# Optimization experiments

Measured on AMD Instinct MI355X. Metric: run time of the kernel, lower is better.

The kernel has to match this reference:

```python
import jax, jax.numpy as jnp
import numpy as np

B, TP, TH = 128, 128, 64
V, E, H, O = 50000, 300, 512, 3


def _lstm(x, lens, Wih, Whh, bih, bhh):
    # PyTorch LSTM, batch_first, gate order i,f,g,o; masked like pack_padded_sequence
    Bn, T, _ = x.shape
    Hn = Whh.shape[1]
    mask = jnp.arange(T)[None, :] < lens[:, None]  # [B,T]
    def step(carry, xt_mt):
        h, c = carry
        xt, mt = xt_mt  # [B,E], [B,1]
        g = xt @ Wih.T + h @ Whh.T + bih + bhh
        i, f, gg, o = jnp.split(g, 4, axis=-1)
        c_new = jax.nn.sigmoid(f) * c + jax.nn.sigmoid(i) * jnp.tanh(gg)
        h_new = jax.nn.sigmoid(o) * jnp.tanh(c_new)
        return (jnp.where(mt, h_new, h), jnp.where(mt, c_new, c)), jnp.where(mt, h_new, 0.0)
    z = jnp.zeros((Bn, Hn), x.dtype)
    _, hs = jax.lax.scan(step, (z, z), (jnp.swapaxes(x, 0, 1), jnp.swapaxes(mask, 0, 1)[..., None]))
    return jnp.swapaxes(hs, 0, 1)  # [B,T,H]


def _cell(x, h, c, Wih, Whh, bih, bhh):
    g = x @ Wih.T + h @ Whh.T + bih + bhh
    i, f, gg, o = jnp.split(g, 4, axis=-1)
    c_new = jax.nn.sigmoid(f) * c + jax.nn.sigmoid(i) * jnp.tanh(gg)
    h_new = jax.nn.sigmoid(o) * jnp.tanh(c_new)
    return h_new, c_new


def setup_inputs() -> dict:
    key = jax.random.key(0)
    ks = jax.random.split(key, 24)
    def unif(k, shape, fan):
        s = 1.0 / np.sqrt(fan)
        return jax.random.uniform(k, shape, jnp.float32, -s, s)
    inp = {}
    inp["premise"] = jax.random.randint(ks[0], (B, TP), 0, V, jnp.int32)
    inp["premise_len"] = jnp.full((B,), TP, jnp.int32)
    inp["hypothesis"] = jax.random.randint(ks[1], (B, TH), 0, V, jnp.int32)
    inp["hypothesis_len"] = jnp.full((B,), TH, jnp.int32)
    inp["embed_table"] = jax.random.normal(ks[2], (V, E), jnp.float32) * 0.1
    inp["embed_table"] = inp["embed_table"].at[0].set(0.0)  # padding_idx=0
    # premise LSTM
    inp["Wih_p"] = unif(ks[3], (4 * H, E), H); inp["Whh_p"] = unif(ks[4], (4 * H, H), H)
    inp["bih_p"] = unif(ks[5], (4 * H,), H); inp["bhh_p"] = unif(ks[6], (4 * H,), H)
    # hypothesis LSTM
    inp["Wih_h"] = unif(ks[7], (4 * H, E), H); inp["Whh_h"] = unif(ks[8], (4 * H, H), H)
    inp["bih_h"] = unif(ks[9], (4 * H,), H); inp["bhh_h"] = unif(ks[10], (4 * H,), H)
    # match LSTMCell (input 2H)
    inp["Wih_m"] = unif(ks[11], (4 * H, 2 * H), H); inp["Whh_m"] = unif(ks[12], (4 * H, H), H)
    inp["bih_m"] = unif(ks[13], (4 * H,), H); inp["bhh_m"] = unif(ks[14], (4 * H,), H)
    # attention
    inp["w_e"] = jax.random.uniform(ks[15], (H,), jnp.float32, 0.0, 1.0)
    inp["W_s"] = unif(ks[16], (H, H), H)
    inp["W_t"] = unif(ks[17], (H, H), H)
    inp["W_m"] = unif(ks[18], (H, H), H)
    inp["W_fc"] = unif(ks[19], (O, H), H)
    inp["b_fc"] = unif(ks[20], (O,), H)
    return inp


def reference(premise, premise_len, hypothesis, hypothesis_len, embed_table,
              Wih_p, Whh_p, bih_p, bhh_p, Wih_h, Whh_h, bih_h, bhh_h,
              Wih_m, Whh_m, bih_m, bhh_m, w_e, W_s, W_t, W_m, W_fc, b_fc):
    Bn = premise.shape[0]
    Hn = Whh_m.shape[1]
    p_emb = embed_table[premise]      # [B,Tp,E]
    h_emb = embed_table[hypothesis]   # [B,Th,E]
    h_s = _lstm(p_emb, premise_len, Wih_p, Whh_p, bih_p, bhh_p)      # [B,Tp,H]
    h_t = _lstm(h_emb, hypothesis_len, Wih_h, Whh_h, bih_h, bhh_h)   # [B,Th,H]
    Ws = jnp.einsum('bth,gh->btg', h_s, W_s)  # precompute w_s(h_s) once

    def step(carry, htk):
        h_m, c_m = carry
        q = htk @ W_t.T + h_m @ W_m.T                    # [B,H]
        s = jnp.tanh(Ws + q[:, None, :])                 # [B,Tp,H]
        e = s @ w_e                                      # [B,Tp]
        alpha = jax.nn.softmax(e, axis=1)                # softmax over premise positions
        a = jnp.einsum('bt,bth->bh', alpha, h_s)
        m_k = jnp.concatenate([a, htk], axis=1)          # [B,2H]
        h_m2, c_m2 = _cell(m_k, h_m, c_m, Wih_m, Whh_m, bih_m, bhh_m)
        return (h_m2, c_m2), h_m2

    z = jnp.zeros((Bn, Hn), h_s.dtype)
    _, hm_all = jax.lax.scan(step, (z, z), jnp.swapaxes(h_t, 0, 1))  # [Th,B,H]
    hm_all = jnp.swapaxes(hm_all, 0, 1)                              # [B,Th,H]
    idx = (hypothesis_len - 1).astype(jnp.int32)[:, None, None]
    last = jnp.take_along_axis(hm_all, idx, axis=1)[:, 0, :]         # last hidden per example
    return last @ W_fc.T + b_fc
```

## Files before the change

kernel.cpp:

```cpp
#include <hip/hip_runtime.h>
#include <hip/hip_bf16.h>

constexpr int BB = 128;
constexpr int TPp = 128;
constexpr int THh = 64;
constexpr int HH = 512;

constexpr size_t OFF_HS     = 0;
constexpr size_t SZ_HS      = (size_t)16384 * 512;
constexpr size_t OFF_HT     = OFF_HS + SZ_HS;
constexpr size_t SZ_HT      = (size_t)8192 * 512;
constexpr size_t OFF_WSM    = OFF_HT + SZ_HT;
constexpr size_t SZ_WSM     = (size_t)16384 * 512;
constexpr size_t OFF_XG_P   = OFF_WSM;
constexpr size_t OFF_XG_H   = OFF_WSM + (size_t)16 * 128 * 128 * 16;
constexpr size_t OFF_WIHT_P = OFF_WSM + SZ_WSM;
constexpr size_t SZ_WIHT    = (size_t)304 * 2048;
constexpr size_t OFF_WIHT_H = OFF_WIHT_P + SZ_WIHT;
constexpr size_t OFF_WHHT_P = OFF_WIHT_H + SZ_WIHT;
constexpr size_t OFF_WHHT_H = OFF_WHHT_P + (size_t)512 * 2048;
constexpr size_t OFF_WB1T   = OFF_WHHT_H + (size_t)512 * 2048;
constexpr size_t OFF_WIA    = OFF_WB1T + (size_t)2560 * 1024;
constexpr size_t OFF_WEF    = OFF_WIA + (size_t)2048 * 512;
constexpr size_t OFF_BM     = OFF_WEF + 512;
constexpr size_t OFF_HC_P   = OFF_BM + 2048;
constexpr size_t OFF_HC_H   = OFF_HC_P + 2 * (size_t)BB * HH;
constexpr size_t OFF_C_P    = OFF_HC_H + 2 * (size_t)BB * HH;
constexpr size_t OFF_C_H    = OFF_C_P + (size_t)BB * HH;
constexpr size_t OFF_Q      = OFF_C_H + (size_t)BB * HH;
constexpr size_t OFF_GH     = OFF_Q + (size_t)BB * HH;
constexpr size_t OFF_A      = OFF_GH + (size_t)BB * 2048;
constexpr size_t OFF_HM     = OFF_A + (size_t)BB * HH;
constexpr size_t OFF_CM     = OFF_HM + (size_t)BB * HH;
constexpr size_t OFF_LAST   = OFF_CM + (size_t)BB * HH;
constexpr size_t OFF_BARP   = OFF_LAST + (size_t)BB * HH;
constexpr size_t OFF_BARH   = OFF_BARP + 2560;
constexpr size_t OFF_BARF   = OFF_BARH + 2560;
constexpr size_t OFF_BARM   = OFF_BARF + 4352;
constexpr size_t WS_FLOATS  = OFF_BARM + 4352;

__device__ __forceinline__ float sigmf(float x) { return 1.0f / (1.0f + __expf(-x)); }
__device__ __forceinline__ float tanh_f(float x) {
  float e = __expf(-2.0f * fabsf(x));
  float r = (1.0f - e) / (1.0f + e);
  return copysignf(r, x);
}

__device__ __forceinline__ void gbarN(unsigned* bar, int ep, int base, int n) {
  __syncthreads();
  const int tid = threadIdx.x;
  const int rel = (int)blockIdx.x - base;
  if (tid == 0) {
    __threadfence();
    __hip_atomic_store(bar + (size_t)rel * 16, (unsigned)ep,
                       __ATOMIC_RELAXED, __HIP_MEMORY_SCOPE_AGENT);
  }
  if (rel == 0) {
    for (int s = tid; s < n; s += (int)blockDim.x) {
      while (__hip_atomic_load(bar + (size_t)s * 16,
                               __ATOMIC_RELAXED, __HIP_MEMORY_SCOPE_AGENT) < (unsigned)ep)
        __builtin_amdgcn_s_sleep(1);
    }
    __syncthreads();
    if (tid == 0)
      __hip_atomic_store(bar + (size_t)n * 16, (unsigned)ep,
                         __ATOMIC_RELAXED, __HIP_MEMORY_SCOPE_AGENT);
  } else if (tid == 0) {
    while (__hip_atomic_load(bar + (size_t)n * 16,
                             __ATOMIC_RELAXED, __HIP_MEMORY_SCOPE_AGENT) < (unsigned)ep)
      __builtin_amdgcn_s_sleep(1);
  }
  if (tid == 0) __threadfence();
  __syncthreads();
}

__global__ void k_diag(float* out, float v) {
  int i = blockIdx.x * 64 + threadIdx.x;
  if (i < BB * 3) out[i] = v;
}

__global__ __launch_bounds__(256) void k_prep(float* ws,
    const float* Wih_p, const float* bih_p, const float* bhh_p,
    const float* Wih_h, const float* bih_h, const float* bhh_h,
    const float* Whh_p, const float* Whh_h,
    const float* Whh_m, const float* Wih_m, const float* bih_m, const float* bhh_m,
    const float* W_m, const float* W_t, const float* w_e) {
  size_t gid = (size_t)blockIdx.x * 256 + threadIdx.x;
  if (gid < SZ_WIHT) {
    int k = (int)(gid >> 11), r = (int)(gid & 2047);
    float v = (k < 300) ? Wih_p[(size_t)r * 300 + k]
            : (k == 303) ? (bih_p[r] + bhh_p[r]) : 0.f;
    ws[OFF_WIHT_P + gid] = v;
    return;
  }
  gid -= SZ_WIHT;
  if (gid < SZ_WIHT) {
    int k = (int)(gid >> 11), r = (int)(gid & 2047);
    float v = (k < 300) ? Wih_h[(size_t)r * 300 + k]
            : (k == 303) ? (bih_h[r] + bhh_h[r]) : 0.f;
    ws[OFF_WIHT_H + gid] = v;
    return;
  }
  gid -= SZ_WIHT;
  const size_t NT = (size_t)512 * 2048;
  if (gid < NT) {
    int li = (int)(gid >> 13);
    int rem = (int)(gid & 8191);
    int k = rem >> 4, c = rem & 15;
    int jj = c >> 2, g = c & 3;
    ws[OFF_WHHT_P + gid] = Whh_p[(size_t)(g * 512 + li * 4 + jj) * 512 + k];
    return;
  }
  gid -= NT;
  if (gid < NT) {
    int li = (int)(gid >> 13);
    int rem = (int)(gid & 8191);
    int k = rem >> 4, c = rem & 15;
    int jj = c >> 2, g = c & 3;
    ws[OFF_WHHT_H + gid] = Whh_h[(size_t)(g * 512 + li * 4 + jj) * 512 + k];
    return;
  }
  gid -= NT;
  if (gid < (size_t)2560 * 1024) {
    int c = (int)(gid >> 10), k = (int)(gid & 1023);
    float v;
    if (c < 512) {
      v = (k < 512) ? W_m[(size_t)c * 512 + k] : W_t[(size_t)c * 512 + (k - 512)];
    } else {
      int p = c - 512;
      int j = p >> 2, g = p & 3;
      int r = g * 512 + j;
      v = (k < 512) ? Whh_m[(size_t)r * 512 + k] : Wih_m[(size_t)r * 1024 + k];
    }
    ws[OFF_WB1T + gid] = v;
    return;
  }
  gid -= (size_t)2560 * 1024;
  if (gid < (size_t)2048 * 512) {
    int c = (int)(gid >> 9), k = (int)(gid & 511);
    int j = c >> 2, g = c & 3;
    ws[OFF_WIA + gid] = Wih_m[((size_t)g * 512 + j) * 1024 + k];
    return;
  }
  gid -= (size_t)2048 * 512;
  if (gid < 512) { ws[OFF_WEF + gid] = w_e[gid]; return; }
  gid -= 512;
  if (gid < 2048) { ws[OFF_BM + gid] = bih_m[gid] + bhh_m[gid]; return; }
  gid -= 2048;
  if (gid < (size_t)393216) { ws[OFF_HC_P + gid] = 0.f; return; }
  gid -= 393216;
  if (gid < (size_t)131072) { ws[OFF_HM + gid] = 0.f; return; }
  gid -= 131072;
  if (gid < 11824) { ws[OFF_BARP + gid] = 0.f; return; }
}

__global__ __launch_bounds__(256) void k_gemm(const float* __restrict__ A,
                                              const float* __restrict__ Bw, int ldb, int Kdim,
                                              int N, float* __restrict__ C, int ntilesN) {
  __shared__ float As[16][68];
  __shared__ float Bs[16][68];
  const int tid = threadIdx.x;
  const int bid = blockIdx.x;
  const int tm = bid / ntilesN, tn = bid % ntilesN;
  const int m0 = tm * 64, n0 = tn * 64;
  const int tx = tid & 15, ty = tid >> 4;
  const int srow = tid >> 2, skc = (tid & 3) * 4;
  float acc[4][4] = {};
  const float* arowf = A + (size_t)(m0 + srow) * Kdim;
  const float* brow = Bw + (size_t)(n0 + srow) * ldb;
  for (int k0 = 0; k0 < Kdim; k0 += 16) {
    float4 v = *(const float4*)(arowf + k0 + skc);
    As[skc + 0][srow] = v.x; As[skc + 1][srow] = v.y;
    As[skc + 2][srow] = v.z; As[skc + 3][srow] = v.w;
#pragma unroll
    for (int i = 0; i < 4; i++) Bs[skc + i][srow] = brow[k0 + skc + i];
    __syncthreads();
#pragma unroll
    for (int kk = 0; kk < 16; kk++) {
      float4 a4 = *(float4*)&As[kk][ty * 4];
      float4 b4 = *(float4*)&Bs[kk][tx * 4];
      acc[0][0] += a4.x * b4.x; acc[0][1] += a4.x * b4.y; acc[0][2] += a4.x * b4.z; acc[0][3] += a4.x * b4.w;
      acc[1][0] += a4.y * b4.x; acc[1][1] += a4.y * b4.y; acc[1][2] += a4.y * b4.z; acc[1][3] += a4.y * b4.w;
      acc[2][0] += a4.z * b4.x; acc[2][1] += a4.z * b4.y; acc[2][2] += a4.z * b4.z; acc[2][3] += a4.z * b4.w;
      acc[3][0] += a4.w * b4.x; acc[3][1] += a4.w * b4.y; acc[3][2] += a4.w * b4.z; acc[3][3] += a4.w * b4.w;
    }
    __syncthreads();
  }
  const int m = m0 + ty * 4, n = n0 + tx * 4;
#pragma unroll
  for (int i = 0; i < 4; i++) {
    float4 o = {acc[i][0], acc[i][1], acc[i][2], acc[i][3]};
    *(float4*)&C[(size_t)(m + i) * N + n] = o;
  }
}

__global__ __launch_bounds__(512, 2) void k_lstm_mega(float* __restrict__ ws,
    const int* __restrict__ premise, const int* __restrict__ hyp,
    const int* __restrict__ plen, const int* __restrict__ hlen,
    const float* __restrict__ emb) {
  __shared__ float4 smem4[4096];
  float4* wlds4 = smem4;
  float4* hbuf4 = smem4 + 2048;
  float* xAs = (float*)(smem4 + 2048);
  float* xBs = xAs + 16 * 68;
  int* xTok = (int*)(xBs + 16 * 68);

  const int tid = threadIdx.x;
  const int bid = blockIdx.x;
  const int seq = bid >> 7;
  const int li = bid & 127;
  const int T = seq ? THh : TPp;
  const int* lens = seq ? hlen : plen;
  const float* wstk = ws + (seq ? OFF_WHHT_H : OFF_WHHT_P) + (size_t)li * 8192;
  float* hsout = ws + (seq ? OFF_HT : OFF_HS);
  float* hc = ws + (seq ? OFF_HC_H : OFF_HC_P);
  unsigned* barS = (unsigned*)(ws + (seq ? OFF_BARH : OFF_BARP));
  unsigned* barF = (unsigned*)(ws + OFF_BARF);
  const int sbase = seq ? 128 : 0;

  {
    const float4* src = (const float4*)wstk;
#pragma unroll
    for (int j2 = 0; j2 < 4; j2++) wlds4[tid + j2 * 512] = src[tid + j2 * 512];
  }
  const int w = tid >> 6, lane = tid & 63;
  const int cg = w & 3, bh = w >> 2;
  const int b = bh * 64 + lane;
  const int sw = b & 7;
  const int jcol = li * 4 + cg;
  const int len = lens[b];
  float c_r = 0.f, h_r = 0.f;
  int epS = 1, epF = 1;

  int sb[4], sk[4];
#pragma unroll
  for (int j2 = 0; j2 < 4; j2++) { int fi = tid + j2 * 512; sb[j2] = fi >> 4; sk[j2] = fi & 15; }

  for (int t = 0; t < TPp; t++) {
    if ((t & 15) == 0) {
      if (t > 0) { gbarN(barF, epF, 0, 256); epF++; }
      int ntl = (t < THh) ? 2048 : 1024;
      __syncthreads();
      for (int tile = bid; tile < ntl; tile += 256) {
        const int seqx = tile >> 10;
        const int u = tile & 1023;
        const int tm = u >> 5, tn = u & 31;
        const int m0 = tm * 64, n0 = tn * 64;
        const int Tx = seqx ? THh : TPp;
        const int* toks = seqx ? hyp : premise;
        const float* WX = ws + (seqx ? OFF_WIHT_H : OFF_WIHT_P);
        float* xg = ws + (seqx ? OFF_XG_H : OFF_XG_P);
        if (tid < 64) {
          int rr = m0 + tid;
          int tl = rr >> 7, bb = rr & 127;
          xTok[tid] = toks[(size_t)bb * Tx + t + tl];
        }
        __syncthreads();
        const int sr = tid & 63;
        const int sk2 = (tid >> 6) * 2;
        const int tx = tid & 15, ty = tid >> 4;
        float acc2[2][4] = {};
        for (int k0 = 0; k0 < 304; k0 += 16) {
          int tok = xTok[sr];
#pragma unroll
          for (int i = 0; i < 2; i++) {
            int kx = k0 + sk2 + i;
            float v = 0.f;
            if (kx < 300) v = emb[(size_t)tok * 300 + kx];
            else if (kx == 303) v = 1.0f;
            xAs[(sk2 + i) * 68 + sr] = v;
          }
#pragma unroll
          for (int s = 0; s < 2; s++) {
            int i2 = tid + s * 512;
            int kb = i2 >> 6, nb = i2 & 63;
            xBs[kb * 68 + nb] = WX[(size_t)(k0 + kb) * 2048 + n0 + nb];
          }
          __syncthreads();
#pragma unroll
          for (int kk = 0; kk < 16; kk++) {
            float a0 = xAs[kk * 68 + ty * 2];
            float a1 = xAs[kk * 68 + ty * 2 + 1];
            float4 b4 = *(float4*)&xBs[kk * 68 + tx * 4];
            acc2[0][0] += a0 * b4.x; acc2[0][1] += a0 * b4.y; acc2[0][2] += a0 * b4.z; acc2[0][3] += a0 * b4.w;
            acc2[1][0] += a1 * b4.x; acc2[1][1] += a1 * b4.y; acc2[1][2] += a1 * b4.z; acc2[1][3] += a1 * b4.w;
          }
          __syncthreads();
        }
        const int cbase = n0 + tx * 4;
        const int g = cbase >> 9;
        const int li2 = (cbase & 511) >> 2;
#pragma unroll
        for (int i = 0; i < 2; i++) {
          int rr = m0 + ty * 2 + i;
          int tl = rr >> 7, brow = rr & 127;
          float* dst = xg + (((size_t)tl * 128 + li2) * 128 + brow) * 16 + g;
#pragma unroll
          for (int jj = 0; jj < 4; jj++) dst[jj * 4] = acc2[i][jj];
        }
      }
      gbarN(barF, epF, 0, 256); epF++;
    }
    if (!(seq && t >= THh)) {
      const int par = t & 1;
      const float* hin = hc + (size_t)par * (BB * HH);
      float* hout = hc + (size_t)(par ^ 1) * (BB * HH);
      const float* xgp = ws + (seq ? OFF_XG_H : OFF_XG_P) + ((size_t)(t & 15) * 128 + li) * 2048;
      float4 acc = {0.f, 0.f, 0.f, 0.f};
      float4 pre[4];
#pragma unroll
      for (int j2 = 0; j2 < 4; j2++)
        pre[j2] = *(const float4*)(hin + (size_t)sb[j2] * 512 + sk[j2] * 4);
      for (int kc = 0; kc < 512; kc += 64) {
        __syncthreads();
#pragma unroll
        for (int j2 = 0; j2 < 4; j2++)
          hbuf4[sb[j2] * 16 + (sk[j2] ^ (sb[j2] & 7))] = pre[j2];
        __syncthreads();
        if (kc + 64 < 512) {
#pragma unroll
          for (int j2 = 0; j2 < 4; j2++)
            pre[j2] = *(const float4*)(hin + (size_t)sb[j2] * 512 + (kc + 64) + sk[j2] * 4);
        }
#pragma unroll
        for (int kk = 0; kk < 64; kk += 4) {
          int k4 = kk >> 2;
          float4 h4 = hbuf4[b * 16 + (k4 ^ sw)];
          float4 w0 = wlds4[(kc + kk + 0) * 4 + cg];
          float4 w1 = wlds4[(kc + kk + 1) * 4 + cg];
          float4 w2 = wlds4[(kc + kk + 2) * 4 + cg];
          float4 w3 = wlds4[(kc + kk + 3) * 4 + cg];
          acc.x += h4.x * w0.x + h4.y * w1.x + h4.z * w2.x + h4.w * w3.x;
          acc.y += h4.x * w0.y + h4.y * w1.y + h4.z * w2.y + h4.w * w3.y;
          acc.z += h4.x * w0.z + h4.y * w1.z + h4.z * w2.z + h4.w * w3.z;
          acc.w += h4.x * w0.w + h4.y * w1.w + h4.z * w2.w + h4.w * w3.w;
        }
      }
      float4 x0 = *(const float4*)(xgp + (size_t)b * 16 + cg * 4);
      float iv = sigmf(acc.x + x0.x), fv = sigmf(acc.y + x0.y);
      float gv = tanh_f(acc.z + x0.z), ov = sigmf(acc.w + x0.w);
      float cn = fv * c_r + iv * gv;
      float hn = ov * tanh_f(cn);
      bool inr = t < len;
      if (inr) { c_r = cn; h_r = hn; }
      hsout[((size_t)b * T + t) * 512 + jcol] = inr ? hn : 0.f;
      hout[(size_t)b * 512 + jcol] = h_r;
      gbarN(barS, epS, sbase, 128); epS++;
    }
  }
}

__global__ __launch_bounds__(512, 2) void k_match_mega(float* __restrict__ ws,
                                                       const int* __restrict__ hlen) {
  __shared__ float smem[16384];
  float* B1 = smem;
  float* DYN = smem + 10240;
  float4* AL1 = (float4*)DYN;
  float* P1P = DYN + 4096;
  float* W3 = DYN;
  float4* AL3 = (float4*)(DYN + 4096);
  float* P3P = DYN + 4096;
  float* q_lds = DYN; float* we_lds = DYN + 512; float* e_part = DYN + 1024;
  float* e_lds = DYN + 1536; float* alpha_lds = DYN + 1664; float* red_s = DYN + 1792;

  const int tid = threadIdx.x;
  const int bid = blockIdx.x;
  float* hm = ws + OFF_HM;
  const float* ht = ws + OFF_HT;
  float* qT = ws + OFF_Q;
  float* ghT = ws + OFF_GH;
  float* abuf = ws + OFF_A;
  float* last = ws + OFF_LAST;
  unsigned* barM = (unsigned*)(ws + OFF_BARM);

  {
    const float* wb1t = ws + OFF_WB1T + (size_t)bid * 10 * 1024;
    for (int i = tid; i < 10 * 1024; i += 512) B1[i] = wb1t[i];
  }
  const int w = tid >> 6, lane = tid & 63;
  const int h5 = w >> 2;
  const int khh = (w >> 1) & 1;
  const int rh = w & 1;
  const int r = rh * 64 + lane;
  const int jh = h5;
  const int j3 = bid * 2 + jh;
  const int i0 = tid, i1 = tid + 512;
  const int kh0s = i0 >> 9, b0s = (i0 & 511) >> 2, q0s = i0 & 3;
  const int kh1s = i1 >> 9, b1s = (i1 & 511) >> 2, q1s = i1 & 3;
  const int idx0 = kh0s * 512 + q0s * 128 + b0s;
  const int idx1 = kh1s * 512 + q1s * 128 + b1s;
  const int kh3s = tid >> 8, b3s = (tid & 255) >> 1, q3s = tid & 1;
  const int idx3 = kh3s * 256 + q3s * 128 + b3s;
  float c_reg = 0.f;
  float bmp[4];
#pragma unroll
  for (int g = 0; g < 4; g++) bmp[g] = ws[OFF_BM + g * 512 + j3];
  const int hl = hlen[r];
  int ep = 1;
  __syncthreads();

  for (int k = 0; k < THh; k++) {
    {
      float acc1[5] = {0.f, 0.f, 0.f, 0.f, 0.f};
      float4 p0, p1;
      p0 = (kh0s == 0) ? *(const float4*)&hm[(size_t)b0s * 512 + q0s * 4]
                       : *(const float4*)&ht[((size_t)b0s * THh + k) * 512 + q0s * 4];
      p1 = (kh1s == 0) ? *(const float4*)&hm[(size_t)b1s * 512 + q1s * 4]
                       : *(const float4*)&ht[((size_t)b1s * THh + k) * 512 + q1s * 4];
      for (int ch = 0; ch < 32; ch++) {
        __syncthreads();
        AL1[idx0] = p0;
        AL1[idx1] = p1;
        __syncthreads();
        if (ch < 31) {
          int kn = (ch + 1) * 16;
          p0 = (kh0s == 0) ? *(const float4*)&hm[(size_t)b0s * 512 + kn + q0s * 4]
                           : *(const float4*)&ht[((size_t)b0s * THh + k) * 512 + kn + q0s * 4];
          p1 = (kh1s == 0) ? *(const float4*)&hm[(size_t)b1s * 512 + kn + q1s * 4]
                           : *(const float4*)&ht[((size_t)b1s * THh + k) * 512 + kn + q1s * 4];
        }
        const int kc = ch * 16;
        const int cb = h5 * 5;
        const int kbase = khh * 512 + kc;
#pragma unroll
        for (int kk4 = 0; kk4 < 4; kk4++) {
          float4 av = AL1[khh * 512 + kk4 * 128 + r];
#pragma unroll
          for (int cc = 0; cc < 5; cc++) {
            float4 bv = *(float4*)&B1[(cb + cc) * 1024 + kbase + kk4 * 4];
            acc1[cc] += av.x * bv.x + av.y * bv.y + av.z * bv.z + av.w * bv.w;
          }
        }
      }
      __syncthreads();
      if (khh == 1) {
#pragma unroll
        for (int cc = 0; cc < 5; cc++) P1P[((size_t)h5 * 128 + r) * 5 + cc] = acc1[cc];
      }
      __syncthreads();
      if (khh == 0) {
        const int cbase = bid * 10 + h5 * 5;
#pragma unroll
        for (int cc = 0; cc < 5; cc++) {
          float val = acc1[cc] + P1P[((size_t)h5 * 128 + r) * 5 + cc];
          int c = cbase + cc;
          if (c < 512) qT[(size_t)c * 128 + r] = val;
          else ghT[(size_t)(c - 512) * 128 + r] = val;
        }
      }
    }
    gbarN(barM, ep, 0, 256); ep++;
    if (bid < 128) {
      const int b = bid;
      const float* Wsb = ws + OFF_WSM;
      const float* hs = ws + OFF_HS;
      const float* wef = ws + OFF_WEF;
      q_lds[tid] = qT[(size_t)tid * 128 + b];
      we_lds[tid] = wef[tid];
      __syncthreads();
      {
        int t2 = tid >> 2;
        int gbase = (tid & 3) * 128;
        const float* wsrow = Wsb + ((size_t)b * TPp + t2) * 512 + gbase;
        float s = 0.f;
        for (int ii = 0; ii < 128; ii += 4) {
          float4 wv = *(const float4*)(wsrow + ii);
          float4 qv = *(float4*)&q_lds[gbase + ii];
          float4 ev = *(float4*)&we_lds[gbase + ii];
          s += tanh_f(wv.x + qv.x) * ev.x + tanh_f(wv.y + qv.y) * ev.y +
               tanh_f(wv.z + qv.z) * ev.z + tanh_f(wv.w + qv.w) * ev.w;
        }
        e_part[tid] = s;
      }
      __syncthreads();
      if (tid < 128)
        e_lds[tid] = e_part[tid * 4] + e_part[tid * 4 + 1] + e_part[tid * 4 + 2] + e_part[tid * 4 + 3];
      __syncthreads();
      if (tid < 64) {
        float m = fmaxf(e_lds[tid], e_lds[tid + 64]);
        for (int off = 32; off > 0; off >>= 1) m = fmaxf(m, __shfl_down(m, off));
        if (tid == 0) red_s[0] = m;
      }
      __syncthreads();
      if (tid < 128) alpha_lds[tid] = __expf(e_lds[tid] - red_s[0]);
      __syncthreads();
      if (tid < 64) {
        float s = alpha_lds[tid] + alpha_lds[tid + 64];
        for (int off = 32; off > 0; off >>= 1) s += __shfl_down(s, off);
        if (tid == 0) red_s[1] = 1.f / s;
      }
      __syncthreads();
      {
        float inv = red_s[1];
        float a0 = 0.f;
        const float* hsb = hs + (size_t)b * TPp * 512 + tid;
        for (int t2 = 0; t2 < TPp; t2++) a0 += alpha_lds[t2] * hsb[(size_t)t2 * 512];
        abuf[(size_t)b * 512 + tid] = a0 * inv;
      }
    }
    gbarN(barM, ep, 0, 256); ep++;
    {
      const float* wiat = ws + OFF_WIA + (size_t)bid * 8 * 512;
#pragma unroll
      for (int s = 0; s < 8; s++) W3[tid + s * 512] = wiat[tid + s * 512];
      float acc3[4] = {0.f, 0.f, 0.f, 0.f};
      float4 p3 = *(const float4*)&abuf[(size_t)b3s * 512 + kh3s * 256 + q3s * 4];
      for (int ch = 0; ch < 32; ch++) {
        __syncthreads();
        AL3[idx3] = p3;
        __syncthreads();
        if (ch < 31) {
          int kn = (ch + 1) * 8;
          p3 = *(const float4*)&abuf[(size_t)b3s * 512 + kh3s * 256 + kn + q3s * 4];
        }
        const int kc = ch * 8;
#pragma unroll
        for (int kk4 = 0; kk4 < 2; kk4++) {
          float4 av = AL3[khh * 256 + kk4 * 128 + r];
#pragma unroll
          for (int g = 0; g < 4; g++) {
            float4 wv = *(float4*)&W3[(jh * 4 + g) * 512 + khh * 256 + kc + kk4 * 4];
            acc3[g] += av.x * wv.x + av.y * wv.y + av.z * wv.z + av.w * wv.w;
          }
        }
      }
      __syncthreads();
      if (khh == 1) {
#pragma unroll
        for (int g = 0; g < 4; g++) P3P[((size_t)jh * 128 + r) * 4 + g] = acc3[g];
      }
      __syncthreads();
      if (khh == 0) {
        float gi = acc3[0] + P3P[((size_t)jh * 128 + r) * 4 + 0] + ghT[(size_t)(j3 * 4 + 0) * 128 + r] + bmp[0];
        float gf = acc3[1] + P3P[((size_t)jh * 128 + r) * 4 + 1] + ghT[(size_t)(j3 * 4 + 1) * 128 + r] + bmp[1];
        float gg = acc3[2] + P3P[((size_t)jh * 128 + r) * 4 + 2] + ghT[(size_t)(j3 * 4 + 2) * 128 + r] + bmp[2];
        float go = acc3[3] + P3P[((size_t)jh * 128 + r) * 4 + 3] + ghT[(size_t)(j3 * 4 + 3) * 128 + r] + bmp[3];
        float iv = sigmf(gi), fv = sigmf(gf), gv = tanh_f(gg), ov = sigmf(go);
        float cn = fv * c_reg + iv * gv;
        float hn = ov * tanh_f(cn);
        c_reg = cn;
        hm[(size_t)r * 512 + j3] = hn;
        if (k == hl - 1) last[(size_t)r * 512 + j3] = hn;
      }
    }
    gbarN(barM, ep, 0, 256); ep++;
  }
}

__global__ __launch_bounds__(256) void k_fc(const float* __restrict__ ws, const float* __restrict__ Wfc,
                                            const float* __restrict__ bfc, float* __restrict__ out) {
  int idx = blockIdx.x * 256 + threadIdx.x;
  if (idx >= BB * 3) return;
  int b = idx / 3, o = idx - b * 3;
  const float* lrow = ws + OFF_LAST + (size_t)b * 512;
  const float* wrow = Wfc + (size_t)o * 512;
  float acc = bfc[o];
  for (int h = 0; h < 512; h++) acc += lrow[h] * wrow[h];
  out[idx] = acc;
}

extern "C" void kernel_launch(void* const* d_in, const int* in_sizes, int n_in, void* d_out,
                              int out_size, void* d_ws, size_t ws_size, hipStream_t stream) {
  const int* premise = (const int*)d_in[0];
  const int* plen = (const int*)d_in[1];
  const int* hyp = (const int*)d_in[2];
  const int* hlen = (const int*)d_in[3];
  const float* emb = (const float*)d_in[4];
  const float* Wih_p = (const float*)d_in[5];
  const float* Whh_p = (const float*)d_in[6];
  const float* bih_p = (const float*)d_in[7];
  const float* bhh_p = (const float*)d_in[8];
  const float* Wih_h = (const float*)d_in[9];
  const float* Whh_h = (const float*)d_in[10];
  const float* bih_h = (const float*)d_in[11];
  const float* bhh_h = (const float*)d_in[12];
  const float* Wih_m = (const float*)d_in[13];
  const float* Whh_m = (const float*)d_in[14];
  const float* bih_m = (const float*)d_in[15];
  const float* bhh_m = (const float*)d_in[16];
  const float* w_e = (const float*)d_in[17];
  const float* W_s = (const float*)d_in[18];
  const float* W_t = (const float*)d_in[19];
  const float* W_m = (const float*)d_in[20];
  const float* W_fc = (const float*)d_in[21];
  const float* b_fc = (const float*)d_in[22];
  float* ws = (float*)d_ws;
  float* out = (float*)d_out;

  if (ws_size < WS_FLOATS * sizeof(float)) {
    float mb = (float)((double)ws_size / (1024.0 * 1024.0));
    k_diag<<<dim3(6), dim3(64), 0, stream>>>(out, mb);
    return;
  }

  {
    size_t total = 2 * SZ_WIHT + 2 * (size_t)512 * 2048 + (size_t)2560 * 1024 +
                   (size_t)2048 * 512 + 512 + 2048 + 393216 + 131072 + 11824;
    int nb = (int)((total + 255) / 256);
    k_prep<<<dim3(nb), dim3(256), 0, stream>>>(ws, Wih_p, bih_p, bhh_p, Wih_h, bih_h, bhh_h,
                                               Whh_p, Whh_h, Whh_m, Wih_m, bih_m, bhh_m,
                                               W_m, W_t, w_e);
  }
  {
    void* args[] = {(void*)&ws, (void*)&premise, (void*)&hyp, (void*)&plen, (void*)&hlen, (void*)&emb};
    hipError_t e = hipLaunchCooperativeKernel((const void*)k_lstm_mega, dim3(256), dim3(512),
                                              args, 0, stream);
    if (e != hipSuccess)
      k_lstm_mega<<<dim3(256), dim3(512), 0, stream>>>(ws, premise, hyp, plen, hlen, emb);
  }
  k_gemm<<<dim3(256 * 8), dim3(256), 0, stream>>>(ws + OFF_HS, W_s, 512, 512, 512,
                                                  ws + OFF_WSM, 8);
  {
    void* args[] = {(void*)&ws, (void*)&hlen};
    hipError_t e = hipLaunchCooperativeKernel((const void*)k_match_mega, dim3(256), dim3(512),
                                              args, 0, stream);
    if (e != hipSuccess)
      k_match_mega<<<dim3(256), dim3(512), 0, stream>>>(ws, hlen);
  }
  k_fc<<<dim3(2), dim3(256), 0, stream>>>(ws, W_fc, b_fc, out);
}
```

Before: 13.87 ms.

## Localize LSTM input projection per block and shrink match kernel to 128 blocks

```diff
diff --git a/kernel.cpp b/kernel.cpp
--- a/kernel.cpp
+++ b/kernel.cpp
@@ -1,5 +1,4 @@
 #include <hip/hip_runtime.h>
-#include <hip/hip_bf16.h>
 
 constexpr int BB = 128;
 constexpr int TPp = 128;
@@ -12,8 +11,6 @@
 constexpr size_t SZ_HT      = (size_t)8192 * 512;
 constexpr size_t OFF_WSM    = OFF_HT + SZ_HT;
 constexpr size_t SZ_WSM     = (size_t)16384 * 512;
-constexpr size_t OFF_XG_P   = OFF_WSM;
-constexpr size_t OFF_XG_H   = OFF_WSM + (size_t)16 * 128 * 128 * 16;
 constexpr size_t OFF_WIHT_P = OFF_WSM + SZ_WSM;
 constexpr size_t SZ_WIHT    = (size_t)304 * 2048;
 constexpr size_t OFF_WIHT_H = OFF_WIHT_P + SZ_WIHT;
@@ -46,21 +43,36 @@
   return copysignf(r, x);
 }
 
-__device__ __forceinline__ void gbarN(unsigned* bar, int ep, int base, int n) {
+__device__ __forceinline__ float aload4(const float* p) {
+  unsigned u = __hip_atomic_load((const unsigned*)p, __ATOMIC_RELAXED, __HIP_MEMORY_SCOPE_AGENT);
+  return __uint_as_float(u);
+}
+__device__ __forceinline__ void astore4(float* p, float v) {
+  __hip_atomic_store((unsigned*)p, __float_as_uint(v), __ATOMIC_RELAXED, __HIP_MEMORY_SCOPE_AGENT);
+}
+__device__ __forceinline__ float4 aload16(const float* p) {
+  const unsigned long long* q = (const unsigned long long*)p;
+  unsigned long long u0 = __hip_atomic_load(q, __ATOMIC_RELAXED, __HIP_MEMORY_SCOPE_AGENT);
+  unsigned long long u1 = __hip_atomic_load(q + 1, __ATOMIC_RELAXED, __HIP_MEMORY_SCOPE_AGENT);
+  union { unsigned long long u; float2 f; } c0, c1;
+  c0.u = u0; c1.u = u1;
+  float4 f; f.x = c0.f.x; f.y = c0.f.y; f.z = c1.f.x; f.w = c1.f.y;
+  return f;
+}
+
+__device__ __forceinline__ void gbar3(unsigned* bar, int ep, int base, int n) {
+  asm volatile("s_waitcnt vmcnt(0) lgkmcnt(0)" ::: "memory");
   __syncthreads();
   const int tid = threadIdx.x;
   const int rel = (int)blockIdx.x - base;
-  if (tid == 0) {
-    __threadfence();
+  if (tid == 0)
     __hip_atomic_store(bar + (size_t)rel * 16, (unsigned)ep,
                        __ATOMIC_RELAXED, __HIP_MEMORY_SCOPE_AGENT);
-  }
   if (rel == 0) {
-    for (int s = tid; s < n; s += (int)blockDim.x) {
+    for (int s = tid; s < n; s += (int)blockDim.x)
       while (__hip_atomic_load(bar + (size_t)s * 16,
                                __ATOMIC_RELAXED, __HIP_MEMORY_SCOPE_AGENT) < (unsigned)ep)
         __builtin_amdgcn_s_sleep(1);
-    }
     __syncthreads();
     if (tid == 0)
       __hip_atomic_store(bar + (size_t)n * 16, (unsigned)ep,
@@ -70,7 +82,6 @@
                              __ATOMIC_RELAXED, __HIP_MEMORY_SCOPE_AGENT) < (unsigned)ep)
       __builtin_amdgcn_s_sleep(1);
   }
-  if (tid == 0) __threadfence();
   __syncthreads();
 }
 
@@ -151,7 +162,7 @@
   gid -= 393216;
   if (gid < (size_t)131072) { ws[OFF_HM + gid] = 0.f; return; }
   gid -= 131072;
-  if (gid < 11824) { ws[OFF_BARP + gid] = 0.f; return; }
+  if (gid < 13824) { ws[OFF_BARP + gid] = 0.f; return; }
 }
 
 __global__ __launch_bounds__(256) void k_gemm(const float* __restrict__ A,
@@ -194,35 +205,29 @@
   }
 }
 
-__global__ __launch_bounds__(512, 2) void k_lstm_mega(float* __restrict__ ws,
+__global__ __launch_bounds__(512) void k_lstm_mega(float* __restrict__ ws,
     const int* __restrict__ premise, const int* __restrict__ hyp,
     const int* __restrict__ plen, const int* __restrict__ hlen,
     const float* __restrict__ emb) {
-  __shared__ float4 smem4[4096];
-  float4* wlds4 = smem4;
-  float4* hbuf4 = smem4 + 2048;
-  float* xAs = (float*)(smem4 + 2048);
-  float* xBs = xAs + 16 * 68;
-  int* xTok = (int*)(xBs + 16 * 68);
+  __shared__ float4 wlds4[2048];
+  __shared__ float4 scr4[2048];
+  float* Bx = (float*)wlds4;
+  float* Alds = (float*)scr4;
 
   const int tid = threadIdx.x;
   const int bid = blockIdx.x;
   const int seq = bid >> 7;
   const int li = bid & 127;
   const int T = seq ? THh : TPp;
+  const int* toks = seq ? hyp : premise;
   const int* lens = seq ? hlen : plen;
   const float* wstk = ws + (seq ? OFF_WHHT_H : OFF_WHHT_P) + (size_t)li * 8192;
-  float* hsout = ws + (seq ? OFF_HT : OFF_HS);
+  const float* WX = ws + (seq ? OFF_WIHT_H : OFF_WIHT_P);
   float* hc = ws + (seq ? OFF_HC_H : OFF_HC_P);
+  float* xg = ws + OFF_WSM + (size_t)bid * 32768;
   unsigned* barS = (unsigned*)(ws + (seq ? OFF_BARH : OFF_BARP));
-  unsigned* barF = (unsigned*)(ws + OFF_BARF);
   const int sbase = seq ? 128 : 0;
 
-  {
-    const float4* src = (const float4*)wstk;
-#pragma unroll
-    for (int j2 = 0; j2 < 4; j2++) wlds4[tid + j2 * 512] = src[tid + j2 * 512];
-  }
   const int w = tid >> 6, lane = tid & 63;
   const int cg = w & 3, bh = w >> 2;
   const int b = bh * 64 + lane;
@@ -230,102 +235,111 @@
   const int jcol = li * 4 + cg;
   const int len = lens[b];
   float c_r = 0.f, h_r = 0.f;
-  int epS = 1, epF = 1;
-
+  int epS = 1;
   int sb[4], sk[4];
 #pragma unroll
   for (int j2 = 0; j2 < 4; j2++) { int fi = tid + j2 * 512; sb[j2] = fi >> 4; sk[j2] = fi & 15; }
-
-  for (int t = 0; t < TPp; t++) {
+  const int kofs = (tid & 3) * 4;
+
+  for (int t = 0; t < T; t++) {
     if ((t & 15) == 0) {
-      if (t > 0) { gbarN(barF, epF, 0, 256); epF++; }
-      int ntl = (t < THh) ? 2048 : 1024;
-      __syncthreads();
-      for (int tile = bid; tile < ntl; tile += 256) {
-        const int seqx = tile >> 10;
-        const int u = tile & 1023;
-        const int tm = u >> 5, tn = u & 31;
-        const int m0 = tm * 64, n0 = tn * 64;
-        const int Tx = seqx ? THh : TPp;
-        const int* toks = seqx ? hyp : premise;
-        const float* WX = ws + (seqx ? OFF_WIHT_H : OFF_WIHT_P);
-        float* xg = ws + (seqx ? OFF_XG_H : OFF_XG_P);
-        if (tid < 64) {
-          int rr = m0 + tid;
-          int tl = rr >> 7, bb = rr & 127;
-          xTok[tid] = toks[(size_t)bb * Tx + t + tl];
-        }
-        __syncthreads();
-        const int sr = tid & 63;
-        const int sk2 = (tid >> 6) * 2;
-        const int tx = tid & 15, ty = tid >> 4;
-        float acc2[2][4] = {};
-        for (int k0 = 0; k0 < 304; k0 += 16) {
-          int tok = xTok[sr];
-#pragma unroll
-          for (int i = 0; i < 2; i++) {
-            int kx = k0 + sk2 + i;
-            float v = 0.f;
-            if (kx < 300) v = emb[(size_t)tok * 300 + kx];
-            else if (kx == 303) v = 1.0f;
-            xAs[(sk2 + i) * 68 + sr] = v;
-          }
-#pragma unroll
-          for (int s = 0; s < 2; s++) {
-            int i2 = tid + s * 512;
-            int kb = i2 >> 6, nb = i2 & 63;
-            xBs[kb * 68 + nb] = WX[(size_t)(k0 + kb) * 2048 + n0 + nb];
+      __syncthreads();
+      for (int i = tid; i < 16 * 304; i += 512) {
+        int c = i / 304, kk = i - c * 304;
+        int jj = c >> 2, g = c & 3;
+        Bx[i] = WX[(size_t)kk * 2048 + g * 512 + li * 4 + jj];
+      }
+      __syncthreads();
+      for (int rg = 0; rg < 4; rg++) {
+        int tk[4];
+#pragma unroll
+        for (int j2 = 0; j2 < 4; j2++) {
+          int rl = (tid >> 2) + j2 * 128;
+          int R = rg * 512 + rl;
+          int tl = R >> 7, bb = R & 127;
+          tk[j2] = toks[(size_t)bb * T + t + tl];
+        }
+        float4 pa[4];
+#pragma unroll
+        for (int j2 = 0; j2 < 4; j2++) {
+          if (kofs + 3 < 300) pa[j2] = *(const float4*)(emb + (size_t)tk[j2] * 300 + kofs);
+          else { float4 z = {0.f, 0.f, 0.f, 0.f}; pa[j2] = z; }
+        }
+        float acc[16];
+#pragma unroll
+        for (int c = 0; c < 16; c++) acc[c] = 0.f;
+        for (int ck = 0; ck < 19; ck++) {
+          __syncthreads();
+#pragma unroll
+          for (int j2 = 0; j2 < 4; j2++) {
+            int fi = tid + j2 * 512;
+            *(float4*)&Alds[(fi >> 2) * 16 + kofs] = pa[j2];
           }
           __syncthreads();
-#pragma unroll
-          for (int kk = 0; kk < 16; kk++) {
-            float a0 = xAs[kk * 68 + ty * 2];
-            float a1 = xAs[kk * 68 + ty * 2 + 1];
-            float4 b4 = *(float4*)&xBs[kk * 68 + tx * 4];
-            acc2[0][0] += a0 * b4.x; acc2[0][1] += a0 * b4.y; acc2[0][2] += a0 * b4.z; acc2[0][3] += a0 * b4.w;
-            acc2[1][0] += a1 * b4.x; acc2[1][1] += a1 * b4.y; acc2[1][2] += a1 * b4.z; acc2[1][3] += a1 * b4.w;
+          if (ck < 18) {
+            int kb = (ck + 1) * 16 + kofs;
+#pragma unroll
+            for (int j2 = 0; j2 < 4; j2++) {
+              if (kb + 3 < 300) {
+                pa[j2] = *(const float4*)(emb + (size_t)tk[j2] * 300 + kb);
+              } else {
+                float v0 = (kb + 0 < 300) ? emb[(size_t)tk[j2] * 300 + kb + 0] : (kb + 0 == 303 ? 1.f : 0.f);
+                float v1 = (kb + 1 < 300) ? emb[(size_t)tk[j2] * 300 + kb + 1] : (kb + 1 == 303 ? 1.f : 0.f);
+                float v2 = (kb + 2 < 300) ? emb[(size_t)tk[j2] * 300 + kb + 2] : (kb + 2 == 303 ? 1.f : 0.f);
+                float v3 = (kb + 3 < 300) ? emb[(size_t)tk[j2] * 300 + kb + 3] : (kb + 3 == 303 ? 1.f : 0.f);
+                float4 z = {v0, v1, v2, v3}; pa[j2] = z;
+              }
+            }
           }
-          __syncthreads();
-        }
-        const int cbase = n0 + tx * 4;
-        const int g = cbase >> 9;
-        const int li2 = (cbase & 511) >> 2;
-#pragma unroll
-        for (int i = 0; i < 2; i++) {
-          int rr = m0 + ty * 2 + i;
-          int tl = rr >> 7, brow = rr & 127;
-          float* dst = xg + (((size_t)tl * 128 + li2) * 128 + brow) * 16 + g;
-#pragma unroll
-          for (int jj = 0; jj < 4; jj++) dst[jj * 4] = acc2[i][jj];
-        }
-      }
-      gbarN(barF, epF, 0, 256); epF++;
+          int kb0 = ck * 16;
+#pragma unroll
+          for (int kk4 = 0; kk4 < 4; kk4++) {
+            float4 av = *(float4*)&Alds[tid * 16 + kk4 * 4];
+#pragma unroll
+            for (int c = 0; c < 16; c++) {
+              float4 bv = *(float4*)&Bx[c * 304 + kb0 + kk4 * 4];
+              acc[c] += av.x * bv.x + av.y * bv.y + av.z * bv.z + av.w * bv.w;
+            }
+          }
+        }
+        int R = rg * 512 + tid;
+#pragma unroll
+        for (int cq = 0; cq < 4; cq++) {
+          float4 o = {acc[cq * 4], acc[cq * 4 + 1], acc[cq * 4 + 2], acc[cq * 4 + 3]};
+          *(float4*)&xg[(size_t)R * 16 + cq * 4] = o;
+        }
+      }
+      __syncthreads();
+      {
+        const float4* src = (const float4*)wstk;
+#pragma unroll
+        for (int j2 = 0; j2 < 4; j2++) wlds4[tid + j2 * 512] = src[tid + j2 * 512];
+      }
     }
-    if (!(seq && t >= THh)) {
+    {
       const int par = t & 1;
       const float* hin = hc + (size_t)par * (BB * HH);
       float* hout = hc + (size_t)(par ^ 1) * (BB * HH);
-      const float* xgp = ws + (seq ? OFF_XG_H : OFF_XG_P) + ((size_t)(t & 15) * 128 + li) * 2048;
       float4 acc = {0.f, 0.f, 0.f, 0.f};
       float4 pre[4];
 #pragma unroll
       for (int j2 = 0; j2 < 4; j2++)
-        pre[j2] = *(const float4*)(hin + (size_t)sb[j2] * 512 + sk[j2] * 4);
+        pre[j2] = aload16(hin + (size_t)sb[j2] * 512 + sk[j2] * 4);
       for (int kc = 0; kc < 512; kc += 64) {
         __syncthreads();
 #pragma unroll
         for (int j2 = 0; j2 < 4; j2++)
-          hbuf4[sb[j2] * 16 + (sk[j2] ^ (sb[j2] & 7))] = pre[j2];
+          scr4[sb[j2] * 16 + (sk[j2] ^ (sb[j2] & 7))] = pre[j2];
         __syncthreads();
         if (kc + 64 < 512) {
 #pragma unroll
           for (int j2 = 0; j2 < 4; j2++)
-            pre[j2] = *(const float4*)(hin + (size_t)sb[j2] * 512 + (kc + 64) + sk[j2] * 4);
+            pre[j2] = aload16(hin + (size_t)sb[j2] * 512 + (kc + 64) + sk[j2] * 4);
         }
 #pragma unroll
         for (int kk = 0; kk < 64; kk += 4) {
           int k4 = kk >> 2;
-          float4 h4 = hbuf4[b * 16 + (k4 ^ sw)];
+          float4 h4 = scr4[b * 16 + (k4 ^ sw)];
           float4 w0 = wlds4[(kc + kk + 0) * 4 + cg];
           float4 w1 = wlds4[(kc + kk + 1) * 4 + cg];
           float4 w2 = wlds4[(kc + kk + 2) * 4 + cg];
@@ -336,127 +350,118 @@
           acc.w += h4.x * w0.w + h4.y * w1.w + h4.z * w2.w + h4.w * w3.w;
         }
       }
-      float4 x0 = *(const float4*)(xgp + (size_t)b * 16 + cg * 4);
+      float4 x0 = *(const float4*)&xg[(((size_t)(t & 15)) * 128 + b) * 16 + cg * 4];
       float iv = sigmf(acc.x + x0.x), fv = sigmf(acc.y + x0.y);
       float gv = tanh_f(acc.z + x0.z), ov = sigmf(acc.w + x0.w);
       float cn = fv * c_r + iv * gv;
       float hn = ov * tanh_f(cn);
       bool inr = t < len;
       if (inr) { c_r = cn; h_r = hn; }
-      hsout[((size_t)b * T + t) * 512 + jcol] = inr ? hn : 0.f;
-      hout[(size_t)b * 512 + jcol] = h_r;
-      gbarN(barS, epS, sbase, 128); epS++;
+      if (!seq) ws[OFF_HS + ((size_t)b * TPp + t) * 512 + jcol] = inr ? hn : 0.f;
+      else      ws[OFF_HT + ((size_t)t * 512 + jcol) * 128 + b] = inr ? hn : 0.f;
+      astore4(hout + (size_t)b * 512 + jcol, h_r);
+      gbar3(barS, epS, sbase, 128); epS++;
     }
   }
 }
 
-__global__ __launch_bounds__(512, 2) void k_match_mega(float* __restrict__ ws,
-                                                       const int* __restrict__ hlen) {
-  __shared__ float smem[16384];
-  float* B1 = smem;
-  float* DYN = smem + 10240;
-  float4* AL1 = (float4*)DYN;
-  float* P1P = DYN + 4096;
-  float* W3 = DYN;
-  float4* AL3 = (float4*)(DYN + 4096);
-  float* P3P = DYN + 4096;
-  float* q_lds = DYN; float* we_lds = DYN + 512; float* e_part = DYN + 1024;
-  float* e_lds = DYN + 1536; float* alpha_lds = DYN + 1664; float* red_s = DYN + 1792;
-
+__global__ __launch_bounds__(512) void k_match_mega(float* __restrict__ ws,
+                                                    const int* __restrict__ hlen) {
+  __shared__ float smem[8192];
   const int tid = threadIdx.x;
   const int bid = blockIdx.x;
-  float* hm = ws + OFF_HM;
-  const float* ht = ws + OFF_HT;
   float* qT = ws + OFF_Q;
   float* ghT = ws + OFF_GH;
-  float* abuf = ws + OFF_A;
+  float* abufT = ws + OFF_A;
+  float* hmT = ws + OFF_HM;
   float* last = ws + OFF_LAST;
+  const float* B1 = ws + OFF_WB1T;
+  const float* W3 = ws + OFF_WIA;
+  const float* htT = ws + OFF_HT;
   unsigned* barM = (unsigned*)(ws + OFF_BARM);
 
-  {
-    const float* wb1t = ws + OFF_WB1T + (size_t)bid * 10 * 1024;
-    for (int i = tid; i < 10 * 1024; i += 512) B1[i] = wb1t[i];
-  }
-  const int w = tid >> 6, lane = tid & 63;
-  const int h5 = w >> 2;
-  const int khh = (w >> 1) & 1;
-  const int rh = w & 1;
-  const int r = rh * 64 + lane;
-  const int jh = h5;
-  const int j3 = bid * 2 + jh;
-  const int i0 = tid, i1 = tid + 512;
-  const int kh0s = i0 >> 9, b0s = (i0 & 511) >> 2, q0s = i0 & 3;
-  const int kh1s = i1 >> 9, b1s = (i1 & 511) >> 2, q1s = i1 & 3;
-  const int idx0 = kh0s * 512 + q0s * 128 + b0s;
-  const int idx1 = kh1s * 512 + q1s * 128 + b1s;
-  const int kh3s = tid >> 8, b3s = (tid & 255) >> 1, q3s = tid & 1;
-  const int idx3 = kh3s * 256 + q3s * 128 + b3s;
+  const int r = tid & 127;
+  const int cg = tid >> 7;
+  const int j3 = bid * 4 + cg;
   float c_reg = 0.f;
   float bmp[4];
 #pragma unroll
   for (int g = 0; g < 4; g++) bmp[g] = ws[OFF_BM + g * 512 + j3];
   const int hl = hlen[r];
   int ep = 1;
-  __syncthreads();
 
   for (int k = 0; k < THh; k++) {
     {
-      float acc1[5] = {0.f, 0.f, 0.f, 0.f, 0.f};
-      float4 p0, p1;
-      p0 = (kh0s == 0) ? *(const float4*)&hm[(size_t)b0s * 512 + q0s * 4]
-                       : *(const float4*)&ht[((size_t)b0s * THh + k) * 512 + q0s * 4];
-      p1 = (kh1s == 0) ? *(const float4*)&hm[(size_t)b1s * 512 + q1s * 4]
-                       : *(const float4*)&ht[((size_t)b1s * THh + k) * 512 + q1s * 4];
-      for (int ch = 0; ch < 32; ch++) {
-        __syncthreads();
-        AL1[idx0] = p0;
-        AL1[idx1] = p1;
-        __syncthreads();
-        if (ch < 31) {
-          int kn = (ch + 1) * 16;
-          p0 = (kh0s == 0) ? *(const float4*)&hm[(size_t)b0s * 512 + kn + q0s * 4]
-                           : *(const float4*)&ht[((size_t)b0s * THh + k) * 512 + kn + q0s * 4];
-          p1 = (kh1s == 0) ? *(const float4*)&hm[(size_t)b1s * 512 + kn + q1s * 4]
-                           : *(const float4*)&ht[((size_t)b1s * THh + k) * 512 + kn + q1s * 4];
-        }
-        const int kc = ch * 16;
-        const int cb = h5 * 5;
-        const int kbase = khh * 512 + kc;
-#pragma unroll
-        for (int kk4 = 0; kk4 < 4; kk4++) {
-          float4 av = AL1[khh * 512 + kk4 * 128 + r];
-#pragma unroll
-          for (int cc = 0; cc < 5; cc++) {
-            float4 bv = *(float4*)&B1[(cb + cc) * 1024 + kbase + kk4 * 4];
-            acc1[cc] += av.x * bv.x + av.y * bv.y + av.z * bv.z + av.w * bv.w;
+      float acc[20];
+#pragma unroll
+      for (int cc = 0; cc < 20; cc++) acc[cc] = 0.f;
+      const int cbase = bid * 20;
+      if (cg < 2) {
+        const int kbeg = cg * 256;
+        for (int kk = 0; kk < 256; kk += 4) {
+          int kx = kbeg + kk;
+          float a0 = aload4(&hmT[(size_t)(kx + 0) * 128 + r]);
+          float a1 = aload4(&hmT[(size_t)(kx + 1) * 128 + r]);
+          float a2 = aload4(&hmT[(size_t)(kx + 2) * 128 + r]);
+          float a3 = aload4(&hmT[(size_t)(kx + 3) * 128 + r]);
+#pragma unroll
+          for (int cc = 0; cc < 20; cc++) {
+            float4 bv = *(const float4*)&B1[(size_t)(cbase + cc) * 1024 + kx];
+            acc[cc] += a0 * bv.x + a1 * bv.y + a2 * bv.z + a3 * bv.w;
           }
         }
-      }
-      __syncthreads();
-      if (khh == 1) {
-#pragma unroll
-        for (int cc = 0; cc < 5; cc++) P1P[((size_t)h5 * 128 + r) * 5 + cc] = acc1[cc];
-      }
-      __syncthreads();
-      if (khh == 0) {
-        const int cbase = bid * 10 + h5 * 5;
-#pragma unroll
-        for (int cc = 0; cc < 5; cc++) {
-          float val = acc1[cc] + P1P[((size_t)h5 * 128 + r) * 5 + cc];
+      } else {
+        const int kbeg = (cg - 2) * 256;
+        const float* hcol = htT + (size_t)k * 65536;
+        for (int kk = 0; kk < 256; kk += 4) {
+          int kj = kbeg + kk;
+          float a0 = hcol[(size_t)(kj + 0) * 128 + r];
+          float a1 = hcol[(size_t)(kj + 1) * 128 + r];
+          float a2 = hcol[(size_t)(kj + 2) * 128 + r];
+          float a3 = hcol[(size_t)(kj + 3) * 128 + r];
+#pragma unroll
+          for (int cc = 0; cc < 20; cc++) {
+            float4 bv = *(const float4*)&B1[(size_t)(cbase + cc) * 1024 + 512 + kj];
+            acc[cc] += a0 * bv.x + a1 * bv.y + a2 * bv.z + a3 * bv.w;
+          }
+        }
+      }
+      float* P1R = smem;
+      __syncthreads();
+      if (cg & 1) {
+#pragma unroll
+        for (int cc = 0; cc < 20; cc++) P1R[(((cg >> 1) * 20 + cc) << 7) + r] = acc[cc];
+      }
+      __syncthreads();
+      if (!(cg & 1)) {
+#pragma unroll
+        for (int cc = 0; cc < 20; cc++) acc[cc] += P1R[(((cg >> 1) * 20 + cc) << 7) + r];
+      }
+      __syncthreads();
+      if (cg == 2) {
+#pragma unroll
+        for (int cc = 0; cc < 20; cc++) P1R[(cc << 7) + r] = acc[cc];
+      }
+      __syncthreads();
+      if (cg == 0) {
+#pragma unroll
+        for (int cc = 0; cc < 20; cc++) {
+          float val = acc[cc] + P1R[(cc << 7) + r];
           int c = cbase + cc;
-          if (c < 512) qT[(size_t)c * 128 + r] = val;
-          else ghT[(size_t)(c - 512) * 128 + r] = val;
+          if (c < 512) astore4(&qT[(size_t)c * 128 + r], val);
+          else astore4(&ghT[(size_t)(c - 512) * 128 + r], val);
         }
       }
     }
-    gbarN(barM, ep, 0, 256); ep++;
-    if (bid < 128) {
+    gbar3(barM, ep, 0, 128); ep++;
+    {
+      float* q_lds = smem; float* we_lds = smem + 512; float* e_part = smem + 1024;
+      float* e_lds = smem + 1536; float* alpha_lds = smem + 1664; float* red_s = smem + 1792;
       const int b = bid;
       const float* Wsb = ws + OFF_WSM;
       const float* hs = ws + OFF_HS;
-      const float* wef = ws + OFF_WEF;
-      q_lds[tid] = qT[(size_t)tid * 128 + b];
-      we_lds[tid] = wef[tid];
+      q_lds[tid] = aload4(&qT[(size_t)tid * 128 + b]);
+      we_lds[tid] = ws[OFF_WEF + tid];
       __syncthreads();
       {
         int t2 = tid >> 2;
@@ -495,55 +500,48 @@
         float a0 = 0.f;
         const float* hsb = hs + (size_t)b * TPp * 512 + tid;
         for (int t2 = 0; t2 < TPp; t2++) a0 += alpha_lds[t2] * hsb[(size_t)t2 * 512];
-        abuf[(size_t)b * 512 + tid] = a0 * inv;
+        astore4(&abufT[(size_t)tid * 128 + b], a0 * inv);
       }
     }
-    gbarN(barM, ep, 0, 256); ep++;
+    gbar3(barM, ep, 0, 128); ep++;
     {
-      const float* wiat = ws + OFF_WIA + (size_t)bid * 8 * 512;
-#pragma unroll
-      for (int s = 0; s < 8; s++) W3[tid + s * 512] = wiat[tid + s * 512];
-      float acc3[4] = {0.f, 0.f, 0.f, 0.f};
-      float4 p3 = *(const float4*)&abuf[(size_t)b3s * 512 + kh3s * 256 + q3s * 4];
-      for (int ch = 0; ch < 32; ch++) {
-        __syncthreads();
-        AL3[idx3] = p3;
-        __syncthreads();
-        if (ch < 31) {
-          int kn = (ch + 1) * 8;
-          p3 = *(const float4*)&abuf[(size_t)b3s * 512 + kh3s * 256 + kn + q3s * 4];
-        }
-        const int kc = ch * 8;
-#pragma unroll
-        for (int kk4 = 0; kk4 < 2; kk4++) {
-          float4 av = AL3[khh * 256 + kk4 * 128 + r];
-#pragma unroll
-          for (int g = 0; g < 4; g++) {
-            float4 wv = *(float4*)&W3[(jh * 4 + g) * 512 + khh * 256 + kc + kk4 * 4];
-            acc3[g] += av.x * wv.x + av.y * wv.y + av.z * wv.z + av.w * wv.w;
-          }
-        }
-      }
-      __syncthreads();
-      if (khh == 1) {
-#pragma unroll
-        for (int g = 0; g < 4; g++) P3P[((size_t)jh * 128 + r) * 4 + g] = acc3[g];
-      }
-      __syncthreads();
-      if (khh == 0) {
-        float gi = acc3[0] + P3P[((size_t)jh * 128 + r) * 4 + 0] + ghT[(size_t)(j3 * 4 + 0) * 128 + r] + bmp[0];
-        float gf = acc3[1] + P3P[((size_t)jh * 128 + r) * 4 + 1] + ghT[(size_t)(j3 * 4 + 1) * 128 + r] + bmp[1];
-        float gg = acc3[2] + P3P[((size_t)jh * 128 + r) * 4 + 2] + ghT[(size_t)(j3 * 4 + 2) * 128 + r] + bmp[2];
-        float go = acc3[3] + P3P[((size_t)jh * 128 + r) * 4 + 3] + ghT[(size_t)(j3 * 4 + 3) * 128 + r] + bmp[3];
-        float iv = sigmf(gi), fv = sigmf(gf), gv = tanh_f(gg), ov = sigmf(go);
-        float cn = fv * c_reg + iv * gv;
-        float hn = ov * tanh_f(cn);
-        c_reg = cn;
-        hm[(size_t)r * 512 + j3] = hn;
-        if (k == hl - 1) last[(size_t)r * 512 + j3] = hn;
-      }
+      float acc3[16];
+#pragma unroll
+      for (int cl = 0; cl < 16; cl++) acc3[cl] = 0.f;
+      const int cb = bid * 16;
+      for (int kk = 0; kk < 128; kk += 4) {
+        int kx = cg * 128 + kk;
+        float a0 = aload4(&abufT[(size_t)(kx + 0) * 128 + r]);
+        float a1 = aload4(&abufT[(size_t)(kx + 1) * 128 + r]);
+        float a2 = aload4(&abufT[(size_t)(kx + 2) * 128 + r]);
+        float a3 = aload4(&abufT[(size_t)(kx + 3) * 128 + r]);
+#pragma unroll
+        for (int cl = 0; cl < 16; cl++) {
+          float4 wv = *(const float4*)&W3[(size_t)(cb + cl) * 512 + kx];
+          acc3[cl] += a0 * wv.x + a1 * wv.y + a2 * wv.z + a3 * wv.w;
+        }
+      }
+      float* P3R = smem;
+      __syncthreads();
+#pragma unroll
+      for (int cl = 0; cl < 16; cl++) P3R[((cg * 16 + cl) << 7) + r] = acc3[cl];
+      __syncthreads();
+      float g4[4];
+#pragma unroll
+      for (int g = 0; g < 4; g++) {
+        int cl = cg * 4 + g;
+        float s = P3R[((0 * 16 + cl) << 7) + r] + P3R[((1 * 16 + cl) << 7) + r] +
+                  P3R[((2 * 16 + cl) << 7) + r] + P3R[((3 * 16 + cl) << 7) + r];
+        g4[g] = s + aload4(&ghT[(size_t)(j3 * 4 + g) * 128 + r]) + bmp[g];
+      }
+      float iv = sigmf(g4[0]), fv = sigmf(g4[1]), gg = tanh_f(g4[2]), ov = sigmf(g4[3]);
+      float cn = fv * c_reg + iv * gg;
+      float hn = ov * tanh_f(cn);
+      c_reg = cn;
+      astore4(&hmT[(size_t)j3 * 128 + r], hn);
+      if (k == hl - 1) last[(size_t)r * 512 + j3] = hn;
     }
-    gbarN(barM, ep, 0, 256); ep++;
+    gbar3(barM, ep, 0, 128); ep++;
   }
 }
 
@@ -595,7 +593,7 @@
 
   {
     size_t total = 2 * SZ_WIHT + 2 * (size_t)512 * 2048 + (size_t)2560 * 1024 +
-                   (size_t)2048 * 512 + 512 + 2048 + 393216 + 131072 + 11824;
+                   (size_t)2048 * 512 + 512 + 2048 + 393216 + 131072 + 13824;
     int nb = (int)((total + 255) / 256);
     k_prep<<<dim3(nb), dim3(256), 0, stream>>>(ws, Wih_p, bih_p, bhh_p, Wih_h, bih_h, bhh_h,
                                                Whh_p, Whh_h, Whh_m, Wih_m, bih_m, bhh_m,
@@ -612,10 +610,10 @@
                                                   ws + OFF_WSM, 8);
   {
     void* args[] = {(void*)&ws, (void*)&hlen};
-    hipError_t e = hipLaunchCooperativeKernel((const void*)k_match_mega, dim3(256), dim3(512),
+    hipError_t e = hipLaunchCooperativeKernel((const void*)k_match_mega, dim3(128), dim3(512),
                                               args, 0, stream);
     if (e != hipSuccess)
-      k_match_mega<<<dim3(256), dim3(512), 0, stream>>>(ws, hlen);
+      k_match_mega<<<dim3(128), dim3(512), 0, stream>>>(ws, hlen);
   }
   k_fc<<<dim3(2), dim3(256), 0, stream>>>(ws, W_fc, b_fc, out);
 }
```

Result: slower. 15.55 ms (+12.1%).
